# Optimization experiments

Hardware: AMD Instinct MI355X
Metric: run time of the kernel (lower is better)

## Reference

```python
import jax, jax.numpy as jnp
import numpy as np

INPUT_SIZE = 1
HIDDEN = 30
B, T = 8192, 512


def setup_inputs() -> dict:
    key = jax.random.key(0)
    ks = jax.random.split(key, 7)
    s_ih = 1.0 / np.sqrt(HIDDEN)
    batch = jax.random.normal(ks[0], (B, T, INPUT_SIZE), dtype=jnp.float32)
    # PyTorch LSTM params: gate order i, f, g, o stacked along first dim (4H)
    W_ih = jax.random.uniform(ks[1], (4 * HIDDEN, INPUT_SIZE), minval=-s_ih, maxval=s_ih, dtype=jnp.float32)
    W_hh = jax.random.uniform(ks[2], (4 * HIDDEN, HIDDEN), minval=-s_ih, maxval=s_ih, dtype=jnp.float32)
    b_ih = jax.random.uniform(ks[3], (4 * HIDDEN,), minval=-s_ih, maxval=s_ih, dtype=jnp.float32)
    b_hh = jax.random.uniform(ks[4], (4 * HIDDEN,), minval=-s_ih, maxval=s_ih, dtype=jnp.float32)
    W_fc = jax.random.uniform(ks[5], (1, HIDDEN), minval=-s_ih, maxval=s_ih, dtype=jnp.float32)
    b_fc = jax.random.uniform(ks[6], (1,), minval=-s_ih, maxval=s_ih, dtype=jnp.float32)
    return {"batch": batch, "W_ih": W_ih, "W_hh": W_hh, "b_ih": b_ih, "b_hh": b_hh, "W_fc": W_fc, "b_fc": b_fc}


def _lstm_final_h(x, W_ih, W_hh, b_ih, b_hh):
    # x: [B, T, I] -> final hidden state h_T: [B, H]
    Bx = x.shape[0]
    H = W_hh.shape[1]
    # Precompute input-side gate projections for all timesteps: [T, B, 4H]
    xg = jnp.einsum('bti,gi->tbg', x, W_ih) + (b_ih + b_hh)

    def step(carry, xt):
        h, c = carry
        gates = xt + h @ W_hh.T  # [B, 4H]
        i, f, g, o = jnp.split(gates, 4, axis=-1)
        i = jax.nn.sigmoid(i)
        f = jax.nn.sigmoid(f)
        g = jnp.tanh(g)
        o = jax.nn.sigmoid(o)
        c = f * c + i * g
        h = o * jnp.tanh(c)
        return (h, c), None

    h0 = jnp.zeros((Bx, H), dtype=x.dtype)
    c0 = jnp.zeros((Bx, H), dtype=x.dtype)
    (hT, _), _ = jax.lax.scan(step, (h0, c0), xg)
    return hT


def reference(batch, W_ih, W_hh, b_ih, b_hh, W_fc, b_fc):
    hT = _lstm_final_h(batch, W_ih, W_hh, b_ih, b_hh)  # [B, H]
    out = hT @ W_fc.T + b_fc  # [B, 1]
    return out.squeeze(-1)  # [B]
```

## Files before the change

kernel.cpp:

```cpp
#include <hip/hip_runtime.h>

#define HID 30
#define TS  512
#define NB  16
#define LOG2E 1.44269504088896340736f
#define XSTR 17

typedef __attribute__((ext_vector_type(8))) short bf16x8;
typedef __attribute__((ext_vector_type(4))) float f32x4;

__device__ __forceinline__ float rcp_f(float x){ return __builtin_amdgcn_rcpf(x); }
__device__ __forceinline__ float ex2_f(float x){ return __builtin_amdgcn_exp2f(x); }

__global__ __launch_bounds__(512, 4)
void lstm_mfma_u1b(const float* __restrict__ batch,
                   const float* __restrict__ W_ih,
                   const float* __restrict__ W_hh,
                   const float* __restrict__ b_ih,
                   const float* __restrict__ b_hh,
                   const float* __restrict__ W_fc,
                   const float* __restrict__ b_fc,
                   float* __restrict__ out)
{
    __shared__ int xs[TS * XSTR];
    __shared__ __align__(16) short hhi[2][4][NB][8];
    __shared__ __align__(16) short hlo[2][4][NB][8];

    const int tid  = threadIdx.x;
    const int w    = tid >> 6;
    const int lane = tid & 63;
    const int q    = lane >> 4;
    const int col  = lane & 15;
    const int b0   = blockIdx.x * NB;
    const int u4   = 4 * w + q;
    const int g    = u4 >> 3;
    const int s    = u4 & 7;

    #pragma unroll 4
    for (int i = 0; i < NB; ++i) {
        const float v = batch[(size_t)(b0 + i) * TS + tid];
        const __bf16 xh = (__bf16)v;
        const __bf16 xl = (__bf16)(v - (float)xh);
        xs[tid * XSTR + i] =
            (int)((unsigned)__builtin_bit_cast(unsigned short, xh) |
                 ((unsigned)__builtin_bit_cast(unsigned short, xl) << 16));
    }
    for (int i = tid; i < 2 * 4 * NB * 8 / 2; i += 512) {
        ((int*)hhi)[i] = 0;
        ((int*)hlo)[i] = 0;
    }
    __syncthreads();
    if (tid < NB) {
        const unsigned xp0 = (unsigned)xs[0 * XSTR + tid];
        hhi[0][3][tid][6] = (short)0x3F80;  hlo[0][3][tid][6] = 0;
        hhi[0][3][tid][7] = (short)(xp0 & 0xFFFFu);
        hlo[0][3][tid][7] = (short)(xp0 >> 16);
    }

    bf16x8 ahi, alo;
    {
        const int gate = col & 3;
        const int unit = 4 * w + (col >> 2);
        const float sG = (gate == 2) ? (-2.0f * LOG2E) : (-LOG2E);
        const int R = gate * HID + unit;
        #pragma unroll
        for (int jj = 0; jj < 8; ++jj) {
            const int kk = q * 8 + jj;
            float wv = 0.0f;
            if (unit < HID) {
                if (kk < HID)      wv = W_hh[R * HID + kk];
                else if (kk == 30) wv = b_ih[R] + b_hh[R];
                else               wv = W_ih[R];
            }
            wv *= sG;
            const __bf16 hi = (__bf16)wv;
            const __bf16 lo = (__bf16)(wv - (float)hi);
            ahi[jj] = (short)__builtin_bit_cast(unsigned short, hi);
            alo[jj] = (short)__builtin_bit_cast(unsigned short, lo);
        }
    }

    __syncthreads();

    const float TWOL = 2.0f * LOG2E;
    float cm = 0.0f;

#define STEP(T, RB, WB)                                                        \
{                                                                              \
    const int4 vhi = *(const int4*)&hhi[RB][q][col][0];                        \
    const int4 vlo = *(const int4*)&hlo[RB][q][col][0];                        \
    const bf16x8 bhi = __builtin_bit_cast(bf16x8, vhi);                        \
    const bf16x8 blo = __builtin_bit_cast(bf16x8, vlo);                        \
    f32x4 a = {0.f, 0.f, 0.f, 0.f};                                            \
    a = __builtin_amdgcn_mfma_f32_16x16x32_bf16(ahi, bhi, a, 0, 0, 0);         \
    a = __builtin_amdgcn_mfma_f32_16x16x32_bf16(ahi, blo, a, 0, 0, 0);         \
    a = __builtin_amdgcn_mfma_f32_16x16x32_bf16(alo, bhi, a, 0, 0, 0);         \
                             \
    const float ei = ex2_f(a[0]), ef = ex2_f(a[1]);                            \
    const float eg = ex2_f(a[2]), eo = ex2_f(a[3]);                            \
    const float P  = (1.0f + ei) * (1.0f + eg);                                \
    const float Q  = 1.0f + ef;                                                \
    const float m1 = (eg - 1.0f) * Q;                                          \
    const float num = fmaf(TWOL, m1, cm * P);                                  \
    cm = num * rcp_f(P * Q);                                                   \
    const float e = ex2_f(cm);                                                 \
    const float h = (1.0f - e) * rcp_f((1.0f + e) * (1.0f + eo));              \
    const __bf16 hh = (__bf16)h;                                               \
    const __bf16 hl = (__bf16)(h - (float)hh);                                 \
    unsigned hhs = (unsigned)__builtin_bit_cast(unsigned short, hh);           \
    unsigned hls = (unsigned)__builtin_bit_cast(unsigned short, hl);           \
    if (w == 7) {    \
        const unsigned xp =                                                    \
            (unsigned)xs[((((T) + 1) & (TS - 1))) * XSTR + col];               \
        const bool q2 = (q == 2), q3 = (q == 3);                               \
        hhs = q2 ? 0x3F80u : (q3 ? (xp & 0xFFFFu) : hhs);                      \
        hls = q2 ? 0u      : (q3 ? (xp >> 16)     : hls);                      \
    }                                                                          \
    hhi[WB][g][col][s] = (short)hhs;                                           \
    hlo[WB][g][col][s] = (short)hls;                                           \
    __syncthreads();                                                           \
}

    for (int t2 = 0; t2 < TS / 2; ++t2) {
        STEP(2 * t2,     0, 1)
        STEP(2 * t2 + 1, 1, 0)
    }
#undef STEP

    if (tid < NB) {
        float acc = b_fc[0];
        #pragma unroll
        for (int u = 0; u < HID; ++u) {
            const float hv =
                (float)__builtin_bit_cast(__bf16, (unsigned short)hhi[0][u >> 3][tid][u & 7]) +
                (float)__builtin_bit_cast(__bf16, (unsigned short)hlo[0][u >> 3][tid][u & 7]);
            acc = fmaf(hv, W_fc[u], acc);
        }
        out[b0 + tid] = acc;
    }
}

extern "C" void kernel_launch(void* const* d_in, const int* in_sizes, int n_in,
                              void* d_out, int out_size, void* d_ws, size_t ws_size,
                              hipStream_t stream) {
    const float* batch = (const float*)d_in[0];
    const float* W_ih  = (const float*)d_in[1];
    const float* W_hh  = (const float*)d_in[2];
    const float* b_ih  = (const float*)d_in[3];
    const float* b_hh  = (const float*)d_in[4];
    const float* W_fc  = (const float*)d_in[5];
    const float* b_fc  = (const float*)d_in[6];
    float* out = (float*)d_out;

    const int blocks = 8192 / NB;
    lstm_mfma_u1b<<<blocks, 512, 0, stream>>>(batch, W_ih, W_hh, b_ih, b_hh,
                                              W_fc, b_fc, out);
}
```

Baseline: 200.3 us.

## Apply input projection as scalar FMA and split MFMA chain into two accumulators

Moves the x_t*W_ih term out of the MFMA K-dimension. It is now applied as a per-lane fp32 FMA after the matrix product, and x is stored as plain fp32 in LDS instead of bf16 hi/lo pairs. The three dependent MFMAs become two independent chains (alo*bhi then ahi*bhi, plus ahi*blo) that are summed afterwards. This shortens the serial MFMA latency on the recurrent critical path and removes the wave-7 x injection and select logic. In exchange each step does an extra LDS read and a few adds. The bias slot stays constant at 1.0 in both buffers, and lanes for the padding units skip the h store.

```diff
diff --git a/kernel.cpp b/kernel.cpp
--- a/kernel.cpp
+++ b/kernel.cpp
@@ -13,7 +13,7 @@
 __device__ __forceinline__ float ex2_f(float x){ return __builtin_amdgcn_exp2f(x); }
 
 __global__ __launch_bounds__(512, 4)
-void lstm_mfma_u1b(const float* __restrict__ batch,
+void lstm_mfma_u1d(const float* __restrict__ batch,
                    const float* __restrict__ W_ih,
                    const float* __restrict__ W_hh,
                    const float* __restrict__ b_ih,
@@ -22,7 +22,7 @@
                    const float* __restrict__ b_fc,
                    float* __restrict__ out)
 {
-    __shared__ int xs[TS * XSTR];
+    __shared__ float xs[TS * XSTR];
     __shared__ __align__(16) short hhi[2][4][NB][8];
     __shared__ __align__(16) short hlo[2][4][NB][8];
 
@@ -37,24 +37,16 @@
     const int s    = u4 & 7;
 
     #pragma unroll 4
-    for (int i = 0; i < NB; ++i) {
-        const float v = batch[(size_t)(b0 + i) * TS + tid];
-        const __bf16 xh = (__bf16)v;
-        const __bf16 xl = (__bf16)(v - (float)xh);
-        xs[tid * XSTR + i] =
-            (int)((unsigned)__builtin_bit_cast(unsigned short, xh) |
-                 ((unsigned)__builtin_bit_cast(unsigned short, xl) << 16));
-    }
+    for (int i = 0; i < NB; ++i)
+        xs[tid * XSTR + i] = batch[(size_t)(b0 + i) * TS + tid];
+
     for (int i = tid; i < 2 * 4 * NB * 8 / 2; i += 512) {
         ((int*)hhi)[i] = 0;
         ((int*)hlo)[i] = 0;
     }
     __syncthreads();
-    if (tid < NB) {
-        const unsigned xp0 = (unsigned)xs[0 * XSTR + tid];
-        hhi[0][3][tid][6] = (short)0x3F80;  hlo[0][3][tid][6] = 0;
-        hhi[0][3][tid][7] = (short)(xp0 & 0xFFFFu);
-        hlo[0][3][tid][7] = (short)(xp0 >> 16);
+    if (tid < 2 * NB) {
+        hhi[tid >> 4][3][tid & 15][6] = (short)0x3F80;
     }
 
     bf16x8 ahi, alo;
@@ -70,7 +62,6 @@
             if (unit < HID) {
                 if (kk < HID)      wv = W_hh[R * HID + kk];
                 else if (kk == 30) wv = b_ih[R] + b_hh[R];
-                else               wv = W_ih[R];
             }
             wv *= sG;
             const __bf16 hi = (__bf16)wv;
@@ -80,6 +71,14 @@
         }
     }
 
+    float wx0 = 0.f, wx1 = 0.f, wx2 = 0.f, wx3 = 0.f;
+    if (u4 < HID) {
+        wx0 = W_ih[0 * HID + u4] * (-LOG2E);
+        wx1 = W_ih[1 * HID + u4] * (-LOG2E);
+        wx2 = W_ih[2 * HID + u4] * (-2.0f * LOG2E);
+        wx3 = W_ih[3 * HID + u4] * (-LOG2E);
+    }
+
     __syncthreads();
 
     const float TWOL = 2.0f * LOG2E;
@@ -87,17 +86,22 @@
 
 #define STEP(T, RB, WB)                                                        \
 {                                                                              \
+    const float xv = xs[(T) * XSTR + col];                                     \
     const int4 vhi = *(const int4*)&hhi[RB][q][col][0];                        \
     const int4 vlo = *(const int4*)&hlo[RB][q][col][0];                        \
     const bf16x8 bhi = __builtin_bit_cast(bf16x8, vhi);                        \
     const bf16x8 blo = __builtin_bit_cast(bf16x8, vlo);                        \
-    f32x4 a = {0.f, 0.f, 0.f, 0.f};                                            \
-    a = __builtin_amdgcn_mfma_f32_16x16x32_bf16(ahi, bhi, a, 0, 0, 0);         \
-    a = __builtin_amdgcn_mfma_f32_16x16x32_bf16(ahi, blo, a, 0, 0, 0);         \
-    a = __builtin_amdgcn_mfma_f32_16x16x32_bf16(alo, bhi, a, 0, 0, 0);         \
-                             \
-    const float ei = ex2_f(a[0]), ef = ex2_f(a[1]);                            \
-    const float eg = ex2_f(a[2]), eo = ex2_f(a[3]);                            \
+    const f32x4 z = {0.f, 0.f, 0.f, 0.f};                                      \
+    f32x4 accP = __builtin_amdgcn_mfma_f32_16x16x32_bf16(alo, bhi, z, 0, 0, 0);\
+    f32x4 accQ = __builtin_amdgcn_mfma_f32_16x16x32_bf16(ahi, blo, z, 0, 0, 0);\
+    accP = __builtin_amdgcn_mfma_f32_16x16x32_bf16(ahi, bhi, accP, 0, 0, 0);   \
+                    \
+    const float ai = fmaf(wx0, xv, accP[0] + accQ[0]);                         \
+    const float af = fmaf(wx1, xv, accP[1] + accQ[1]);                         \
+    const float ag = fmaf(wx2, xv, accP[2] + accQ[2]);                         \
+    const float ao = fmaf(wx3, xv, accP[3] + accQ[3]);                         \
+    const float ei = ex2_f(ai), ef = ex2_f(af);                                \
+    const float eg = ex2_f(ag), eo = ex2_f(ao);                                \
     const float P  = (1.0f + ei) * (1.0f + eg);                                \
     const float Q  = 1.0f + ef;                                                \
     const float m1 = (eg - 1.0f) * Q;                                          \
@@ -107,17 +111,10 @@
     const float h = (1.0f - e) * rcp_f((1.0f + e) * (1.0f + eo));              \
     const __bf16 hh = (__bf16)h;                                               \
     const __bf16 hl = (__bf16)(h - (float)hh);                                 \
-    unsigned hhs = (unsigned)__builtin_bit_cast(unsigned short, hh);           \
-    unsigned hls = (unsigned)__builtin_bit_cast(unsigned short, hl);           \
-    if (w == 7) {    \
-        const unsigned xp =                                                    \
-            (unsigned)xs[((((T) + 1) & (TS - 1))) * XSTR + col];               \
-        const bool q2 = (q == 2), q3 = (q == 3);                               \
-        hhs = q2 ? 0x3F80u : (q3 ? (xp & 0xFFFFu) : hhs);                      \
-        hls = q2 ? 0u      : (q3 ? (xp >> 16)     : hls);                      \
+    if (u4 < HID) {      \
+        hhi[WB][g][col][s] = (short)__builtin_bit_cast(unsigned short, hh);    \
+        hlo[WB][g][col][s] = (short)__builtin_bit_cast(unsigned short, hl);    \
     }                                                                          \
-    hhi[WB][g][col][s] = (short)hhs;                                           \
-    hlo[WB][g][col][s] = (short)hls;                                           \
     __syncthreads();                                                           \
 }
 
@@ -153,6 +150,6 @@
     float* out = (float*)d_out;
 
     const int blocks = 8192 / NB;
-    lstm_mfma_u1b<<<blocks, 512, 0, stream>>>(batch, W_ih, W_hh, b_ih, b_hh,
+    lstm_mfma_u1d<<<blocks, 512, 0, stream>>>(batch, W_ih, W_hh, b_ih, b_hh,
                                               W_fc, b_fc, out);
 }
```

Measured after the change: 201.9 us. About the same (+0.8%).
